# Optimization experiments

Measured on AMD Instinct MI355X. Metric: run time of the kernel, lower is better.

Reference implementation:

```python
import jax, jax.numpy as jnp
import numpy as np

N_NODES = 32768
N_EDGES = 524288
NODE_DIM, POS_DIM, EDGE_DIM = 44, 8, 1
HID, OUT, LAYERS, HEADS = 128, 128, 3, 4
DK = HID // HEADS
LN_EPS = 1e-5


def _linear_w(key, fan_in, fan_out):
    return (jax.random.normal(key, (fan_in, fan_out), jnp.float32) / np.sqrt(fan_in)).astype(jnp.float32)


def _ln(x, g, b):
    m = jnp.mean(x, axis=-1, keepdims=True)
    v = jnp.var(x, axis=-1, keepdims=True)
    return (x - m) * jax.lax.rsqrt(v + LN_EPS) * g + b


def setup_inputs() -> dict:
    key = jax.random.key(0)
    ks = jax.random.split(key, 16)
    inp = {
        'feats': jax.random.normal(ks[0], (N_NODES, NODE_DIM), jnp.float32),
        'lap_pos_enc': jax.random.normal(ks[1], (N_NODES, POS_DIM), jnp.float32),
        'edge_feats': jax.random.normal(ks[2], (N_EDGES, EDGE_DIM), jnp.float32),
        'src': jax.random.randint(ks[3], (N_EDGES,), 0, N_NODES, jnp.int32),
        'dst': jax.random.randint(ks[4], (N_EDGES,), 0, N_NODES, jnp.int32),
        # input projections
        'W_node': _linear_w(ks[5], NODE_DIM, HID), 'b_node': jnp.zeros((HID,), jnp.float32),
        'W_pos': _linear_w(ks[6], POS_DIM, HID), 'b_pos': jnp.zeros((HID,), jnp.float32),
        'W_edge': _linear_w(ks[7], EDGE_DIM, HID), 'b_edge': jnp.zeros((HID,), jnp.float32),
    }
    # per-layer stacked params (all layers are HID->HID since OUT==HID)
    def stack(k, fi, fo):
        kk = jax.random.split(k, LAYERS)
        return jnp.stack([_linear_w(kk[i], fi, fo) for i in range(LAYERS)])
    inp['Wq'] = stack(ks[8], HID, HID)
    inp['Wk'] = stack(ks[9], HID, HID)
    inp['Wv'] = stack(ks[10], HID, HID)
    inp['We'] = stack(ks[11], HID, HID)
    inp['W_lin'] = stack(ks[12], HID, HID)
    inp['b_lin'] = jnp.zeros((LAYERS, HID), jnp.float32)
    inp['g1'] = jnp.ones((LAYERS, HID), jnp.float32)
    inp['be1'] = jnp.zeros((LAYERS, HID), jnp.float32)
    inp['Wf1'] = stack(ks[13], HID, 2 * HID)
    inp['bf1'] = jnp.zeros((LAYERS, 2 * HID), jnp.float32)
    inp['Wf2'] = stack(ks[14], 2 * HID, HID)
    inp['bf2'] = jnp.zeros((LAYERS, HID), jnp.float32)
    inp['g2'] = jnp.ones((LAYERS, HID), jnp.float32)
    inp['be2'] = jnp.zeros((LAYERS, HID), jnp.float32)
    return inp


def reference(feats, lap_pos_enc, edge_feats,
              W_node, b_node, W_pos, b_pos, W_edge, b_edge,
              Wq, Wk, Wv, We, W_lin, b_lin, g1, be1,
              Wf1, bf1, Wf2, bf2, g2, be2, src, dst):
    n = feats.shape[0]
    inv_sqrt_dk = np.float32(1.0 / np.sqrt(DK))
    h = feats @ W_node + b_node + lap_pos_enc @ W_pos + b_pos      # [N, HID]
    e = edge_feats @ W_edge + b_edge                               # [E, HID] (shared across layers)
    for i in range(LAYERS):
        Q = (h @ Wq[i]).reshape(n, HEADS, DK)
        K = (h @ Wk[i]).reshape(n, HEADS, DK)
        V = (h @ Wv[i]).reshape(n, HEADS, DK)
        E = (e @ We[i]).reshape(-1, HEADS, DK)                     # [E, H, DK]
        # raw score [E, H, 1] broadcast against (1+E) -> [E, H, DK] (faithful to source)
        score = jnp.sum(K[src] * Q[dst], axis=-1, keepdims=True) * inv_sqrt_dk
        score = score * (1.0 + E)
        alpha = jnp.exp(score)                                      # [E, H, DK]
        Z = jnp.maximum(jax.ops.segment_sum(alpha, dst, num_segments=n), 1e-6)
        h_out = jax.ops.segment_sum(V[src] * alpha, dst, num_segments=n) / Z
        h_out = h_out.reshape(n, HEADS * DK)
        h = h + h_out @ W_lin[i] + b_lin[i]                        # residual + dropout(identity)
        h = _ln(h, g1[i], be1[i])
        h2 = jax.nn.relu(h @ Wf1[i] + bf1[i]) @ Wf2[i] + bf2[i]
        h = _ln(h + h2, g2[i], be2[i])
    # dgl.mean_nodes over a single graph -> [1, OUT]; readout LayerNorm is never applied in source
    return jnp.mean(h, axis=0, keepdims=True)
```

## Files before the change

### kernel.cpp

```cpp
#include <hip/hip_runtime.h>
#include <hip/hip_bf16.h>

#define N_NODES 32768
#define N_EDGES 524288
#define LN_EPS 1e-5f

typedef unsigned short ushort_t;
typedef __attribute__((ext_vector_type(8))) short short8v;
typedef __attribute__((ext_vector_type(4))) float float4v;
typedef __attribute__((ext_vector_type(2))) float float2v;

__device__ __forceinline__ float bf2f(ushort_t u) {
    return __uint_as_float(((unsigned int)u) << 16);
}
__device__ __forceinline__ ushort_t f2bf(float f) {
    unsigned int u = __float_as_uint(f);
    unsigned int r = (u + 0x7FFFu + ((u >> 16) & 1u)) >> 16;
    return (ushort_t)r;
}
__device__ __forceinline__ float lo16(unsigned int x) { return __uint_as_float(x << 16); }
__device__ __forceinline__ float hi16(unsigned int x) { return __uint_as_float(x & 0xFFFF0000u); }

#if __has_builtin(__builtin_amdgcn_exp2f)
#define EXP2(x) __builtin_amdgcn_exp2f(x)
#else
#define EXP2(x) exp2f(x)
#endif

#define OFF_WNODE 0
#define OFF_BNODE 5632
#define OFF_WPOS  5760
#define OFF_BPOS  6784
#define OFF_WEDGE 6912
#define OFF_BEDGE 7040
#define OFF_BLIN  7168
#define OFF_G1    7552
#define OFF_BE1   7936
#define OFF_BF1   8320
#define OFF_BF2   9088
#define OFF_G2    9472
#define OFF_BE2   9856
#define CONV_TOTAL 10240

#define REC_QKV(i)  ((i) * 96)
#define REC_WLIN(i) (288 + (i) * 32)
#define REC_WF1(i)  (384 + (i) * 64)
#define REC_WF2(i)  (576 + (i) * 64)
#define REC_WNP     768
#define REC_TOTAL   784

#define LDS_STRIDE 264
#define LDS_FSTRIDE 132

__global__ void detect_kernel(const unsigned int* __restrict__ wn, int* __restrict__ flag) {
    __shared__ int s[256];
    int t = threadIdx.x;
    int cnt = 0;
    for (int i = t; i < 2816; i += 256) {
        unsigned int b = (wn[i] >> 8) & 0x7F;
        cnt += (b >= 0x3A && b <= 0x40) ? 1 : 0;
    }
    s[t] = cnt;
    __syncthreads();
    for (int off = 128; off > 0; off >>= 1) {
        if (t < off) s[t] += s[t + off];
        __syncthreads();
    }
    if (t == 0) *flag = (s[0] > 1408) ? 1 : 0;
}

struct ConvArgs { const void* src[13]; };

__global__ void convert_kernel(ConvArgs a, const int* __restrict__ flag,
                               float* __restrict__ dst, int* __restrict__ deg) {
    int gid = blockIdx.x * 256 + threadIdx.x;
    for (int i = gid; i < N_NODES; i += CONV_TOTAL) deg[i] = 0;
    if (gid >= CONV_TOTAL) return;
    const int off[14] = {OFF_WNODE, OFF_BNODE, OFF_WPOS, OFF_BPOS, OFF_WEDGE, OFF_BEDGE,
                         OFF_BLIN, OFF_G1, OFF_BE1, OFF_BF1, OFF_BF2, OFF_G2, OFF_BE2,
                         CONV_TOTAL};
    int s = 0;
#pragma unroll
    for (int i = 1; i < 13; ++i) s += (gid >= off[i]) ? 1 : 0;
    int local = gid - off[s];
    if (*flag)
        dst[gid] = bf2f(((const ushort_t*)a.src[s])[local]);
    else
        dst[gid] = ((const float*)a.src[s])[local];
}

__global__ void swz_kernel(const void* __restrict__ Wq, const void* __restrict__ Wk,
                           const void* __restrict__ Wv, const void* __restrict__ Wlin,
                           const void* __restrict__ Wf1, const void* __restrict__ Wf2,
                           const void* __restrict__ We, const void* __restrict__ wedge,
                           const void* __restrict__ bedge,
                           const void* __restrict__ Wn_, const void* __restrict__ Wp_,
                           const int* __restrict__ flag,
                           ushort_t* __restrict__ swz,
                           float* __restrict__ u, float* __restrict__ c1) {
    const bool isbf = (*flag != 0);
    if (blockIdx.x >= 195) {
        int idx = (blockIdx.x - 195) * 256 + threadIdx.x;
        int rec16 = idx >> 6;
        int lane = idx & 63;
        int ct = rec16 >> 1, kb = rec16 & 1;
        int col = lane & 15, quad = lane >> 4;
        int n = ct * 16 + col;
        ushort_t v[8];
#pragma unroll
        for (int j = 0; j < 8; ++j) {
            int k = kb * 32 + quad * 8 + j;
            if (isbf) {
                v[j] = (k < 44) ? ((const ushort_t*)Wn_)[k * 128 + n]
                     : ((k < 52) ? ((const ushort_t*)Wp_)[(k - 44) * 128 + n]
                                 : (ushort_t)0);
            } else {
                float f = (k < 44) ? ((const float*)Wn_)[k * 128 + n]
                        : ((k < 52) ? ((const float*)Wp_)[(k - 44) * 128 + n] : 0.f);
                v[j] = f2bf(f);
            }
        }
        ushort_t* o = swz + (size_t)(REC_WNP + rec16) * 512 + lane * 8;
#pragma unroll
        for (int j = 0; j < 8; ++j) o[j] = v[j];
        return;
    }
    if (blockIdx.x >= 192) {
        int l = blockIdx.x - 192;
        int d = threadIdx.x;
        if (d >= 128) return;
        float uu = 0.f, cc = 0.f;
        if (isbf) {
            const ushort_t* Wl = (const ushort_t*)We + (size_t)l * 16384;
            const ushort_t* we_ = (const ushort_t*)wedge;
            const ushort_t* be_ = (const ushort_t*)bedge;
#pragma unroll 4
            for (int k = 0; k < 128; ++k) {
                float w = bf2f(Wl[k * 128 + d]);
                uu = fmaf(bf2f(we_[k]), w, uu);
                cc = fmaf(bf2f(be_[k]), w, cc);
            }
        } else {
            const float* Wl = (const float*)We + (size_t)l * 16384;
            const float* we_ = (const float*)wedge;
            const float* be_ = (const float*)bedge;
#pragma unroll 4
            for (int k = 0; k < 128; ++k) {
                float w = Wl[k * 128 + d];
                uu = fmaf(we_[k], w, uu);
                cc = fmaf(be_[k], w, cc);
            }
        }
        const float scale = 0.17677669529663687f * 1.4426950408889634f;
        u[l * 128 + d] = uu * scale;
        c1[l * 128 + d] = (1.f + cc) * scale;
        return;
    }
    int gid = blockIdx.x * 256 + threadIdx.x;
    int lane = gid & 63;
    int rec = gid >> 6;
    int col = lane & 15, quad = lane >> 4;
    const void* src;
    size_t base;
    int ct, kb, OC;
    if (rec < 288) {
        int layer = rec / 96, r2 = rec % 96;
        ct = r2 >> 2; kb = r2 & 3;
        int seg = ct >> 3;
        src = (seg == 0) ? Wq : ((seg == 1) ? Wk : Wv);
        base = (size_t)layer * 16384; OC = 128; ct &= 7;
    } else if (rec < 384) {
        int r = rec - 288, layer = r / 32, r2 = r % 32;
        ct = r2 >> 2; kb = r2 & 3;
        src = Wlin; base = (size_t)layer * 16384; OC = 128;
    } else if (rec < 576) {
        int r = rec - 384, layer = r / 64, r2 = r % 64;
        ct = r2 >> 2; kb = r2 & 3;
        src = Wf1; base = (size_t)layer * 32768; OC = 256;
    } else {
        int r = rec - 576, layer = r / 64, r2 = r % 64;
        ct = r2 >> 3; kb = r2 & 7;
        src = Wf2; base = (size_t)layer * 32768; OC = 128;
    }
    int n = ct * 16 + col;
    ushort_t v[8];
    if (isbf) {
        const ushort_t* s16 = (const ushort_t*)src + base;
#pragma unroll
        for (int j = 0; j < 8; ++j) v[j] = s16[(size_t)(kb * 32 + quad * 8 + j) * OC + n];
    } else {
        const float* s32 = (const float*)src + base;
#pragma unroll
        for (int j = 0; j < 8; ++j) v[j] = f2bf(s32[(size_t)(kb * 32 + quad * 8 + j) * OC + n]);
    }
    ushort_t* o = swz + (size_t)rec * 512 + lane * 8;
#pragma unroll
    for (int j = 0; j < 8; ++j) o[j] = v[j];
}

__global__ __launch_bounds__(256) void ip_gemm(
    const void* __restrict__ feats, const void* __restrict__ lap,
    const float* __restrict__ conv, const int* __restrict__ flag,
    const int* __restrict__ dstidx, int* __restrict__ deg,
    const ushort_t* __restrict__ Bswz,
    float* __restrict__ h, ushort_t* __restrict__ hb) {
    __shared__ __align__(16) ushort_t As[64 * 72];
    const int tid = threadIdx.x;

    for (int e = blockIdx.x * 256 + tid; e < N_EDGES; e += (N_NODES / 64) * 256)
        atomicAdd(&deg[dstidx[e]], 1);

    const bool isbf = (*flag != 0);
    const int r = tid >> 2;
    const int t4 = tid & 3;
    const int m0g = blockIdx.x * 64;
    {
        const int row = m0g + r;
        ushort_t tmp[16];
        if (isbf) {
            const ushort_t* frow = (const ushort_t*)feats + (size_t)row * 44;
            const ushort_t* prow = (const ushort_t*)lap + (size_t)row * 8;
#pragma unroll
            for (int j = 0; j < 16; ++j) {
                int k = t4 * 16 + j;
                tmp[j] = (k < 44) ? frow[k]
                       : ((k < 52) ? prow[k - 44] : (ushort_t)0);
            }
        } else {
            const float* frow = (const float*)feats + (size_t)row * 44;
            const float* prow = (const float*)lap + (size_t)row * 8;
#pragma unroll
            for (int j = 0; j < 16; ++j) {
                int k = t4 * 16 + j;
                float v = (k < 44) ? frow[k] : ((k < 52) ? prow[k - 44] : 0.f);
                tmp[j] = f2bf(v);
            }
        }
#pragma unroll
        for (int j = 0; j < 16; ++j) As[r * 72 + t4 * 16 + j] = tmp[j];
    }
    __syncthreads();

    const int wv = tid >> 6, lane = tid & 63;
    const int col = lane & 15, quad = lane >> 4;
    const int m0 = wv * 16;
    short8v a0 = *(const short8v*)&As[(m0 + col) * 72 + quad * 8];
    short8v a1 = *(const short8v*)&As[(m0 + col) * 72 + 32 + quad * 8];

    float4v acc[8];
#pragma unroll
    for (int ct = 0; ct < 8; ++ct) {
        short8v b0 = *(const short8v*)(Bswz + (size_t)(ct * 2 + 0) * 512 + lane * 8);
        short8v b1 = *(const short8v*)(Bswz + (size_t)(ct * 2 + 1) * 512 + lane * 8);
        float4v a = (float4v){0.f, 0.f, 0.f, 0.f};
        a = __builtin_amdgcn_mfma_f32_16x16x32_bf16(a0, b0, a, 0, 0, 0);
        a = __builtin_amdgcn_mfma_f32_16x16x32_bf16(a1, b1, a, 0, 0, 0);
        acc[ct] = a;
    }

    const int rowb = m0g + m0 + quad * 4;
#pragma unroll
    for (int ct = 0; ct < 8; ++ct) {
        int j = ct * 16 + col;
        float bias = conv[OFF_BNODE + j] + conv[OFF_BPOS + j];
#pragma unroll
        for (int rr = 0; rr < 4; ++rr) {
            float o = acc[ct][rr] + bias;
            h[(size_t)(rowb + rr) * 128 + j] = o;
            hb[(size_t)(rowb + rr) * 128 + j] = f2bf(o);
        }
    }
}

__global__ void scan_kernel(const int* __restrict__ deg, int* __restrict__ rowstart,
                            int* __restrict__ cursor, float* __restrict__ macc) {
    __shared__ int lds[1024];
    int t = threadIdx.x;
    if (t < 128) macc[t] = 0.f;
    int base = t * 32;
    int v[32];
    int csum = 0;
#pragma unroll
    for (int j = 0; j < 8; ++j) {
        int4 x = *(const int4*)(deg + base + j * 4);
        v[j * 4 + 0] = x.x; v[j * 4 + 1] = x.y;
        v[j * 4 + 2] = x.z; v[j * 4 + 3] = x.w;
        csum += x.x + x.y + x.z + x.w;
    }
    lds[t] = csum;
    __syncthreads();
    for (int off = 1; off < 1024; off <<= 1) {
        int x = (t >= off) ? lds[t - off] : 0;
        __syncthreads();
        lds[t] += x;
        __syncthreads();
    }
    int excl = lds[t] - csum;
    int running = excl;
#pragma unroll
    for (int j = 0; j < 8; ++j) {
        int4 w;
        w.x = running; running += v[j * 4 + 0];
        w.y = running; running += v[j * 4 + 1];
        w.z = running; running += v[j * 4 + 2];
        w.w = running; running += v[j * 4 + 3];
        *(int4*)(rowstart + base + j * 4) = w;
        *(int4*)(cursor + base + j * 4) = w;
    }
    if (t == 1023) rowstart[N_NODES] = running;
}

__global__ void scatter_kernel(const int* __restrict__ src, const int* __restrict__ dst,
                               const void* __restrict__ ef, const int* __restrict__ flag,
                               int* __restrict__ cursor,
                               unsigned int* __restrict__ edges) {
    int e = blockIdx.x * 256 + threadIdx.x;
    if (e < N_EDGES) {
        ushort_t efb = (*flag != 0) ? ((const ushort_t*)ef)[e]
                                    : f2bf(((const float*)ef)[e]);
        int d = dst[e];
        int p = atomicAdd(&cursor[d], 1);
        edges[p] = (unsigned int)src[e] | ((unsigned int)efb << 16);
    }
}

template <int KB>
__global__ __launch_bounds__(256) void qkv_gemm(
    const ushort_t* __restrict__ A,
    const ushort_t* __restrict__ Bswz,
    ushort_t* __restrict__ outQ,
    unsigned char* __restrict__ outKV) {
    const int K = KB * 32;
    const int tid = threadIdx.x;
    const int wv = tid >> 6, lane = tid & 63;
    const int col = lane & 15, quad = lane >> 4;
    const int m0 = blockIdx.x * 64 + wv * 16;
    const int ct0 = blockIdx.y * 8;

    float4v acc[8];
#pragma unroll
    for (int ct = 0; ct < 8; ++ct) acc[ct] = (float4v){0.f, 0.f, 0.f, 0.f};

    const ushort_t* Ap = A + (size_t)(m0 + col) * K + quad * 8;
    const ushort_t* Bp = Bswz + (size_t)ct0 * KB * 512 + lane * 8;

#pragma unroll
    for (int kb = 0; kb < KB; ++kb) {
        short8v a = *(const short8v*)(Ap + kb * 32);
#pragma unroll
        for (int ct = 0; ct < 8; ++ct) {
            short8v b = *(const short8v*)(Bp + (size_t)(ct * KB + kb) * 512);
            acc[ct] = __builtin_amdgcn_mfma_f32_16x16x32_bf16(a, b, acc[ct], 0, 0, 0);
        }
    }

    const int rowb = m0 + quad * 4;
    const int seg = blockIdx.y;
    if (seg == 0) {
#pragma unroll
        for (int ct = 0; ct < 8; ++ct) {
            int j = ct * 16 + col;
#pragma unroll
            for (int r = 0; r < 4; ++r)
                outQ[(size_t)(rowb + r) * 128 + j] = f2bf(acc[ct][r]);
        }
    } else {
        const int vofs = (seg == 2) ? 8 : 0;
#pragma unroll
        for (int ct = 0; ct < 8; ++ct) {
            int j = ct * 16 + col;
            int off = ((j >> 3) * 16) + (j & 7) + vofs;
#pragma unroll
            for (int r = 0; r < 4; ++r) {
                float a = acc[ct][r];
                float b = __shfl_xor(a, 1, 64);
                if ((col & 1) == 0) {
                    unsigned short pk = (unsigned short)
                        __builtin_amdgcn_cvt_pk_fp8_f32(a, b, 0, false);
                    *(ushort_t*)(outKV + (size_t)(rowb + r) * 256 + off) = pk;
                }
            }
        }
    }
}

__global__ __launch_bounds__(64, 2) void ffn_kernel(
    const ushort_t* __restrict__ HOUT,
    const ushort_t* __restrict__ BWL,
    const ushort_t* __restrict__ BF1,
    const ushort_t* __restrict__ BF2,
    const float* __restrict__ bl,
    const float* __restrict__ g1v, const float* __restrict__ be1v,
    const float* __restrict__ bf1v,
    const float* __restrict__ bf2v,
    const float* __restrict__ g2v, const float* __restrict__ be2v,
    float* __restrict__ h,
    ushort_t* __restrict__ hb) {
    __shared__ __align__(16) char ldsraw[16 * 528];
    ushort_t* ldsu = (ushort_t*)ldsraw;
    float* ldsf = (float*)ldsraw;
    const int lane = threadIdx.x & 63;
    const int col = lane & 15, quad = lane >> 4;
    const int m0 = blockIdx.x * 16;
    const int rowb = m0 + quad * 4;
    const int lrowc = quad * 4;
    const int lrowa = col;

    float4v acc[8];
#pragma unroll
    for (int ct = 0; ct < 8; ++ct) acc[ct] = (float4v){0.f, 0.f, 0.f, 0.f};
    const ushort_t* Ap = HOUT + (size_t)(m0 + col) * 128 + quad * 8;
#pragma unroll
    for (int kb = 0; kb < 4; ++kb) {
        short8v a = *(const short8v*)(Ap + kb * 32);
#pragma unroll
        for (int ct = 0; ct < 8; ++ct) {
            short8v b = *(const short8v*)(BWL + (size_t)(ct * 4 + kb) * 512 + lane * 8);
            acc[ct] = __builtin_amdgcn_mfma_f32_16x16x32_bf16(a, b, acc[ct], 0, 0, 0);
        }
    }

    float val[8][4], s[4] = {0.f, 0.f, 0.f, 0.f}, ss[4] = {0.f, 0.f, 0.f, 0.f};
#pragma unroll
    for (int ct = 0; ct < 8; ++ct) {
        float bi = bl[ct * 16 + col];
#pragma unroll
        for (int r = 0; r < 4; ++r) {
            float v = acc[ct][r] + bi + h[(size_t)(rowb + r) * 128 + ct * 16 + col];
            val[ct][r] = v;
            s[r] += v;
            ss[r] += v * v;
        }
    }
#pragma unroll
    for (int mask = 1; mask < 16; mask <<= 1) {
#pragma unroll
        for (int r = 0; r < 4; ++r) {
            s[r] += __shfl_xor(s[r], mask, 64);
            ss[r] += __shfl_xor(ss[r], mask, 64);
        }
    }
#pragma unroll
    for (int r = 0; r < 4; ++r) {
        float mean = s[r] * (1.f / 128.f);
        float var = ss[r] * (1.f / 128.f) - mean * mean;
        s[r] = mean;
        ss[r] = rsqrtf(var + LN_EPS);
    }
#pragma unroll
    for (int ct = 0; ct < 8; ++ct) {
        float gg = g1v[ct * 16 + col], bb = be1v[ct * 16 + col];
#pragma unroll
        for (int r = 0; r < 4; ++r) {
            float o = (val[ct][r] - s[r]) * ss[r] * gg + bb;
            val[ct][r] = o;
            ldsu[(lrowc + r) * LDS_STRIDE + ct * 16 + col] = f2bf(o);
        }
    }
    __syncthreads();

    short8v af[4];
#pragma unroll
    for (int kb = 0; kb < 4; ++kb)
        af[kb] = *(const short8v*)&ldsu[lrowa * LDS_STRIDE + kb * 32 + quad * 8];

    float4v acc2[16];
#pragma unroll
    for (int ct = 0; ct < 16; ++ct) acc2[ct] = (float4v){0.f, 0.f, 0.f, 0.f};
#pragma unroll
    for (int kb = 0; kb < 4; ++kb) {
#pragma unroll
        for (int ct = 0; ct < 16; ++ct) {
            short8v b = *(const short8v*)(BF1 + (size_t)(ct * 4 + kb) * 512 + lane * 8);
            acc2[ct] = __builtin_amdgcn_mfma_f32_16x16x32_bf16(af[kb], b, acc2[ct], 0, 0, 0);
        }
    }
    __syncthreads();

#pragma unroll
    for (int ct = 0; ct < 16; ++ct) {
        float bi = bf1v[ct * 16 + col];
#pragma unroll
        for (int r = 0; r < 4; ++r) {
            float v = fmaxf(acc2[ct][r] + bi, 0.f);
            ldsu[(lrowc + r) * LDS_STRIDE + ct * 16 + col] = f2bf(v);
        }
    }
    __syncthreads();

    float4v acc3[8];
#pragma unroll
    for (int ct = 0; ct < 8; ++ct) acc3[ct] = (float4v){0.f, 0.f, 0.f, 0.f};
#pragma unroll
    for (int kb = 0; kb < 8; ++kb) {
        short8v a = *(const short8v*)&ldsu[lrowa * LDS_STRIDE + kb * 32 + quad * 8];
#pragma unroll
        for (int ct = 0; ct < 8; ++ct) {
            short8v b = *(const short8v*)(BF2 + (size_t)(ct * 8 + kb) * 512 + lane * 8);
            acc3[ct] = __builtin_amdgcn_mfma_f32_16x16x32_bf16(a, b, acc3[ct], 0, 0, 0);
        }
    }

    float s2[4] = {0.f, 0.f, 0.f, 0.f}, ss2[4] = {0.f, 0.f, 0.f, 0.f};
#pragma unroll
    for (int ct = 0; ct < 8; ++ct) {
        float bi = bf2v[ct * 16 + col];
#pragma unroll
        for (int r = 0; r < 4; ++r) {
            float v = acc3[ct][r] + bi + val[ct][r];
            val[ct][r] = v;
            s2[r] += v;
            ss2[r] += v * v;
        }
    }
#pragma unroll
    for (int mask = 1; mask < 16; mask <<= 1) {
#pragma unroll
        for (int r = 0; r < 4; ++r) {
            s2[r] += __shfl_xor(s2[r], mask, 64);
            ss2[r] += __shfl_xor(ss2[r], mask, 64);
        }
    }
#pragma unroll
    for (int r = 0; r < 4; ++r) {
        float mean = s2[r] * (1.f / 128.f);
        float var = ss2[r] * (1.f / 128.f) - mean * mean;
        s2[r] = mean;
        ss2[r] = rsqrtf(var + LN_EPS);
    }
    __syncthreads();
#pragma unroll
    for (int ct = 0; ct < 8; ++ct) {
        float gg = g2v[ct * 16 + col], bb = be2v[ct * 16 + col];
#pragma unroll
        for (int r = 0; r < 4; ++r) {
            float o = (val[ct][r] - s2[r]) * ss2[r] * gg + bb;
            ldsf[(lrowc + r) * LDS_FSTRIDE + ct * 16 + col] = o;
        }
    }
    __syncthreads();

#pragma unroll
    for (int j = 0; j < 8; ++j) {
        int p = lane + j * 64;
        int row = p >> 5;
        int c4 = p & 31;
        float4 vv = *(const float4*)&ldsf[row * LDS_FSTRIDE + c4 * 4];
        *(float4*)&h[(size_t)(m0 + row) * 128 + c4 * 4] = vv;
    }
#pragma unroll
    for (int j = 0; j < 4; ++j) {
        int p = lane + j * 64;
        int row = p >> 4;
        int c8 = p & 15;
        float4 va = *(const float4*)&ldsf[row * LDS_FSTRIDE + c8 * 8];
        float4 vb = *(const float4*)&ldsf[row * LDS_FSTRIDE + c8 * 8 + 4];
        uint4 ou;
        ou.x = (unsigned)f2bf(va.x) | ((unsigned)f2bf(va.y) << 16);
        ou.y = (unsigned)f2bf(va.z) | ((unsigned)f2bf(va.w) << 16);
        ou.z = (unsigned)f2bf(vb.x) | ((unsigned)f2bf(vb.y) << 16);
        ou.w = (unsigned)f2bf(vb.z) | ((unsigned)f2bf(vb.w) << 16);
        *(uint4*)&hb[(size_t)(m0 + row) * 128 + c8 * 8] = ou;
    }
}

__global__ __launch_bounds__(64) void agg_kernel(
    const ushort_t* __restrict__ Q, const unsigned char* __restrict__ KV,
    const int* __restrict__ rowstart, const unsigned int* __restrict__ edges,
    const float* __restrict__ u, const float* __restrict__ c1,
    ushort_t* __restrict__ hout) {
    const int lane = threadIdx.x & 63;
    const int v = blockIdx.x;
    const int sub = lane & 15;
    const int grp = lane >> 4;

    uint4 qu = *(const uint4*)(Q + (size_t)v * 128 + sub * 8);
    float q0 = lo16(qu.x), q1 = hi16(qu.x), q2 = lo16(qu.y), q3 = hi16(qu.y);
    float q4 = lo16(qu.z), q5 = hi16(qu.z), q6 = lo16(qu.w), q7 = hi16(qu.w);
    float4 uva = *(const float4*)(u + sub * 8);
    float4 uvb = *(const float4*)(u + sub * 8 + 4);
    float4 cva = *(const float4*)(c1 + sub * 8);
    float4 cvb = *(const float4*)(c1 + sub * 8 + 4);

    float m = -1.0e38f;
    float sA[8] = {0.f, 0.f, 0.f, 0.f, 0.f, 0.f, 0.f, 0.f};
    float o[8] = {0.f, 0.f, 0.f, 0.f, 0.f, 0.f, 0.f, 0.f};

    const int start = rowstart[v];
    const int deg = rowstart[v + 1] - start;
    const int nfull = deg >> 2;
    const unsigned int* ep = edges + start + grp;

#define AGG_COMPUTE(PE, KVv, MASKED, VALID)                                      \
    {                                                                            \
        float ef_ = __uint_as_float((PE) & 0xFFFF0000u);                         \
        float2v k01 = __builtin_amdgcn_cvt_pk_f32_fp8((KVv).x, false);           \
        float2v k23 = __builtin_amdgcn_cvt_pk_f32_fp8((KVv).x, true);            \
        float2v k45 = __builtin_amdgcn_cvt_pk_f32_fp8((KVv).y, false);           \
        float2v k67 = __builtin_amdgcn_cvt_pk_f32_fp8((KVv).y, true);            \
        float p_ = k01[0] * q0;                                                  \
        p_ = fmaf(k01[1], q1, p_);                                               \
        p_ = fmaf(k23[0], q2, p_);                                               \
        p_ = fmaf(k23[1], q3, p_);                                               \
        p_ = fmaf(k45[0], q4, p_);                                               \
        p_ = fmaf(k45[1], q5, p_);                                               \
        p_ = fmaf(k67[0], q6, p_);                                               \
        p_ = fmaf(k67[1], q7, p_);                                               \
        p_ += __shfl_xor(p_, 1, 64);                                             \
        p_ += __shfl_xor(p_, 2, 64);                                             \
        float x0 = p_ * fmaf(ef_, uva.x, cva.x);                                 \
        float x1 = p_ * fmaf(ef_, uva.y, cva.y);                                 \
        float x2 = p_ * fmaf(ef_, uva.z, cva.z);                                 \
        float x3 = p_ * fmaf(ef_, uva.w, cva.w);                                 \
        float x4 = p_ * fmaf(ef_, uvb.x, cvb.x);                                 \
        float x5 = p_ * fmaf(ef_, uvb.y, cvb.y);                                 \
        float x6 = p_ * fmaf(ef_, uvb.z, cvb.z);                                 \
        float x7 = p_ * fmaf(ef_, uvb.w, cvb.w);                                 \
        if (MASKED) {                                                            \
            x0 = (VALID) ? x0 : -1.0e38f; x1 = (VALID) ? x1 : -1.0e38f;          \
            x2 = (VALID) ? x2 : -1.0e38f; x3 = (VALID) ? x3 : -1.0e38f;          \
            x4 = (VALID) ? x4 : -1.0e38f; x5 = (VALID) ? x5 : -1.0e38f;          \
            x6 = (VALID) ? x6 : -1.0e38f; x7 = (VALID) ? x7 : -1.0e38f;          \
        }                                                                        \
        float xm = fmaxf(fmaxf(fmaxf(x0, x1), fmaxf(x2, x3)),                    \
                         fmaxf(fmaxf(x4, x5), fmaxf(x6, x7)));                   \
        if (xm > m) {                                                            \
            float nm = xm + 6.0f;                                                \
            float sc = EXP2(m - nm);                                             \
            sA[0] *= sc; sA[1] *= sc; sA[2] *= sc; sA[3] *= sc;                  \
            sA[4] *= sc; sA[5] *= sc; sA[6] *= sc; sA[7] *= sc;                  \
            o[0] *= sc; o[1] *= sc; o[2] *= sc; o[3] *= sc;                      \
            o[4] *= sc; o[5] *= sc; o[6] *= sc; o[7] *= sc;                      \
            m = nm;                                                              \
        }                                                                        \
        float e0 = EXP2(x0 - m), e1 = EXP2(x1 - m);                              \
        float e2 = EXP2(x2 - m), e3 = EXP2(x3 - m);                              \
        float e4 = EXP2(x4 - m), e5 = EXP2(x5 - m);                              \
        float e6 = EXP2(x6 - m), e7 = EXP2(x7 - m);                              \
        sA[0] += e0; sA[1] += e1; sA[2] += e2; sA[3] += e3;                      \
        sA[4] += e4; sA[5] += e5; sA[6] += e6; sA[7] += e7;                      \
        float2v v01 = __builtin_amdgcn_cvt_pk_f32_fp8((KVv).z, false);           \
        float2v v23 = __builtin_amdgcn_cvt_pk_f32_fp8((KVv).z, true);            \
        float2v v45 = __builtin_amdgcn_cvt_pk_f32_fp8((KVv).w, false);           \
        float2v v67 = __builtin_amdgcn_cvt_pk_f32_fp8((KVv).w, true);            \
        o[0] = fmaf(v01[0], e0, o[0]);                                           \
        o[1] = fmaf(v01[1], e1, o[1]);                                           \
        o[2] = fmaf(v23[0], e2, o[2]);                                           \
        o[3] = fmaf(v23[1], e3, o[3]);                                           \
        o[4] = fmaf(v45[0], e4, o[4]);                                           \
        o[5] = fmaf(v45[1], e5, o[5]);                                           \
        o[6] = fmaf(v67[0], e6, o[6]);                                           \
        o[7] = fmaf(v67[1], e7, o[7]);                                           \
    }

    int it = 0;
    for (; it + 4 <= nfull; it += 4) {
        unsigned int pe0 = ep[4 * it];
        unsigned int pe1 = ep[4 * it + 4];
        unsigned int pe2 = ep[4 * it + 8];
        unsigned int pe3 = ep[4 * it + 12];
        uint4 kv0 = *(const uint4*)(KV + (size_t)(pe0 & 0xFFFFu) * 256 + sub * 16);
        uint4 kv1 = *(const uint4*)(KV + (size_t)(pe1 & 0xFFFFu) * 256 + sub * 16);
        uint4 kv2 = *(const uint4*)(KV + (size_t)(pe2 & 0xFFFFu) * 256 + sub * 16);
        uint4 kv3 = *(const uint4*)(KV + (size_t)(pe3 & 0xFFFFu) * 256 + sub * 16);
        AGG_COMPUTE(pe0, kv0, false, true)
        AGG_COMPUTE(pe1, kv1, false, true)
        AGG_COMPUTE(pe2, kv2, false, true)
        AGG_COMPUTE(pe3, kv3, false, true)
    }
    if (it + 2 <= nfull) {
        unsigned int pe0 = ep[4 * it];
        unsigned int pe1 = ep[4 * it + 4];
        uint4 kv0 = *(const uint4*)(KV + (size_t)(pe0 & 0xFFFFu) * 256 + sub * 16);
        uint4 kv1 = *(const uint4*)(KV + (size_t)(pe1 & 0xFFFFu) * 256 + sub * 16);
        AGG_COMPUTE(pe0, kv0, false, true)
        AGG_COMPUTE(pe1, kv1, false, true)
        it += 2;
    }
    if (it < nfull) {
        unsigned int pe0 = ep[4 * it];
        uint4 kv0 = *(const uint4*)(KV + (size_t)(pe0 & 0xFFFFu) * 256 + sub * 16);
        AGG_COMPUTE(pe0, kv0, false, true)
    }
    const int rem = deg & 3;
    if (rem) {
        bool valid = grp < rem;
        unsigned int pe = valid ? ep[4 * nfull] : edges[start];
        uint4 kv = *(const uint4*)(KV + (size_t)(pe & 0xFFFFu) * 256 + sub * 16);
        AGG_COMPUTE(pe, kv, true, valid)
    }
#undef AGG_COMPUTE

#pragma unroll
    for (int mask = 16; mask <= 32; mask <<= 1) {
        float mo = __shfl_xor(m, mask, 64);
        float mm = fmaxf(m, mo);
        float sca = EXP2(m - mm);
        float scb = EXP2(mo - mm);
#pragma unroll
        for (int j = 0; j < 8; ++j) {
            float t = __shfl_xor(sA[j], mask, 64);
            sA[j] = sA[j] * sca + t * scb;
            t = __shfl_xor(o[j], mask, 64);
            o[j] = o[j] * sca + t * scb;
        }
        m = mm;
    }

    if (grp == 0) {
        float zc = 1e-6f * EXP2(-m);
        uint4 ou;
        unsigned int w0, w1;
        float z;
        z = fmaxf(fmaxf(sA[0], zc), 1e-37f); w0 = f2bf(o[0] / z);
        z = fmaxf(fmaxf(sA[1], zc), 1e-37f); w1 = f2bf(o[1] / z);
        ou.x = w0 | (w1 << 16);
        z = fmaxf(fmaxf(sA[2], zc), 1e-37f); w0 = f2bf(o[2] / z);
        z = fmaxf(fmaxf(sA[3], zc), 1e-37f); w1 = f2bf(o[3] / z);
        ou.y = w0 | (w1 << 16);
        z = fmaxf(fmaxf(sA[4], zc), 1e-37f); w0 = f2bf(o[4] / z);
        z = fmaxf(fmaxf(sA[5], zc), 1e-37f); w1 = f2bf(o[5] / z);
        ou.z = w0 | (w1 << 16);
        z = fmaxf(fmaxf(sA[6], zc), 1e-37f); w0 = f2bf(o[6] / z);
        z = fmaxf(fmaxf(sA[7], zc), 1e-37f); w1 = f2bf(o[7] / z);
        ou.w = w0 | (w1 << 16);
        *(uint4*)(hout + (size_t)v * 128 + sub * 8) = ou;
    }
}

__global__ void mean_part_kernel(const float* __restrict__ h, float* __restrict__ macc) {
    __shared__ float s[256];
    int t = threadIdx.x;
    int col = t & 127;
    int half = t >> 7;
    int r0 = blockIdx.x * 256;
    float acc = 0.f;
    for (int r = half; r < 256; r += 2) acc += h[(size_t)(r0 + r) * 128 + col];
    s[t] = acc;
    __syncthreads();
    if (t < 128) atomicAdd(&macc[t], s[t] + s[t + 128]);
}

__global__ void finalize_kernel(const float* __restrict__ macc, void* __restrict__ out,
                                const int* __restrict__ flag) {
    int t = threadIdx.x;
    float v = macc[t] * (1.f / (float)N_NODES);
    if (*flag)
        ((ushort_t*)out)[t] = f2bf(v);
    else
        ((float*)out)[t] = v;
}

extern "C" void kernel_launch(void* const* d_in, const int* in_sizes, int n_in,
                              void* d_out, int out_size, void* d_ws, size_t ws_size,
                              hipStream_t stream) {
    const int* src = (const int*)d_in[3];
    const int* dst = (const int*)d_in[4];

    char* w = (char*)d_ws;
    const size_t MB = 1u << 20;
    float* h        = (float*)(w);
    ushort_t* hb    = (ushort_t*)(w + 16 * MB);
    ushort_t* Qh    = (ushort_t*)(w + 24 * MB);
    unsigned char* KVf8 = (unsigned char*)(w + 32 * MB);
    char* aux       = w + 48 * MB;
    int* deg        = (int*)(aux);
    int* rowstart   = (int*)(aux + 0x40000);
    int* cursor     = (int*)(aux + 0x80000);
    unsigned int* edges = (unsigned int*)(aux + 0xC0000);
    float* ubuf     = (float*)(aux + 0xC0000 + 2 * MB);
    float* cbuf     = ubuf + 3 * 128;
    float* macc     = cbuf + 3 * 128;
    int* flag       = (int*)(macc + 128);
    float* conv     = (float*)(aux + 0xC0000 + 2 * MB + 4096);
    ushort_t* swz   = (ushort_t*)((char*)conv + CONV_TOTAL * 4);

    detect_kernel<<<1, 256, 0, stream>>>((const unsigned int*)d_in[5], flag);

    ConvArgs ca;
    ca.src[0] = d_in[5];
    ca.src[1] = d_in[6];
    ca.src[2] = d_in[7];
    ca.src[3] = d_in[8];
    ca.src[4] = d_in[9];
    ca.src[5] = d_in[10];
    ca.src[6] = d_in[16];
    ca.src[7] = d_in[17];
    ca.src[8] = d_in[18];
    ca.src[9] = d_in[20];
    ca.src[10] = d_in[22];
    ca.src[11] = d_in[23];
    ca.src[12] = d_in[24];
    convert_kernel<<<(CONV_TOTAL + 255) / 256, 256, 0, stream>>>(ca, flag, conv, deg);

    swz_kernel<<<192 + 3 + 4, 256, 0, stream>>>(
        d_in[11], d_in[12], d_in[13], d_in[15], d_in[19], d_in[21],
        d_in[14], d_in[9], d_in[10], d_in[5], d_in[7], flag, swz, ubuf, cbuf);

    ip_gemm<<<N_NODES / 64, 256, 0, stream>>>(d_in[0], d_in[1], conv, flag, dst, deg,
                                              swz + (size_t)REC_WNP * 512, h, hb);
    scan_kernel<<<1, 1024, 0, stream>>>(deg, rowstart, cursor, macc);
    scatter_kernel<<<N_EDGES / 256, 256, 0, stream>>>(src, dst, d_in[2], flag, cursor,
                                                      edges);

    for (int i = 0; i < 3; ++i) {
        const ushort_t* swzQKV = swz + (size_t)REC_QKV(i) * 512;
        const ushort_t* swzWL  = swz + (size_t)REC_WLIN(i) * 512;
        const ushort_t* swzF1  = swz + (size_t)REC_WF1(i) * 512;
        const ushort_t* swzF2  = swz + (size_t)REC_WF2(i) * 512;

        qkv_gemm<4><<<dim3(N_NODES / 64, 3), 256, 0, stream>>>(hb, swzQKV, Qh, KVf8);

        agg_kernel<<<N_NODES, 64, 0, stream>>>(Qh, KVf8, rowstart, edges,
                                               ubuf + i * 128, cbuf + i * 128, hb);

        ffn_kernel<<<N_NODES / 16, 64, 0, stream>>>(
            hb, swzWL, swzF1, swzF2,
            conv + OFF_BLIN + i * 128, conv + OFF_G1 + i * 128, conv + OFF_BE1 + i * 128,
            conv + OFF_BF1 + i * 256,
            conv + OFF_BF2 + i * 128, conv + OFF_G2 + i * 128, conv + OFF_BE2 + i * 128,
            h, hb);
    }

    mean_part_kernel<<<N_NODES / 256, 256, 0, stream>>>(h, macc);
    finalize_kernel<<<1, 128, 0, stream>>>(macc, d_out, flag);
}
```

Before: 475.7 us.

## Ping-pong hidden-state buffers and overlap FFN row tiles with half stride

```diff
diff --git a/kernel.cpp b/kernel.cpp
--- a/kernel.cpp
+++ b/kernel.cpp
@@ -394,14 +394,15 @@
     const float* __restrict__ bf1v,
     const float* __restrict__ bf2v,
     const float* __restrict__ g2v, const float* __restrict__ be2v,
-    float* __restrict__ h,
+    const float* __restrict__ hin,
+    float* __restrict__ hout,
     ushort_t* __restrict__ hb) {
     __shared__ __align__(16) char ldsraw[16 * 528];
     ushort_t* ldsu = (ushort_t*)ldsraw;
     float* ldsf = (float*)ldsraw;
     const int lane = threadIdx.x & 63;
     const int col = lane & 15, quad = lane >> 4;
-    const int m0 = blockIdx.x * 16;
+    const int m0 = blockIdx.x * 8;
     const int rowb = m0 + quad * 4;
     const int lrowc = quad * 4;
     const int lrowa = col;
@@ -426,7 +427,7 @@
         float bi = bl[ct * 16 + col];
 #pragma unroll
         for (int r = 0; r < 4; ++r) {
-            float v = acc[ct][r] + bi + h[(size_t)(rowb + r) * 128 + ct * 16 + col];
+            float v = acc[ct][r] + bi + hin[(size_t)(rowb + r) * 128 + ct * 16 + col];
             val[ct][r] = v;
             s[r] += v;
             ss[r] += v * v;
@@ -546,7 +547,7 @@
         int row = p >> 5;
         int c4 = p & 31;
         float4 vv = *(const float4*)&ldsf[row * LDS_FSTRIDE + c4 * 4];
-        *(float4*)&h[(size_t)(m0 + row) * 128 + c4 * 4] = vv;
+        *(float4*)&hout[(size_t)(m0 + row) * 128 + c4 * 4] = vv;
     }
 #pragma unroll
     for (int j = 0; j < 4; ++j) {
@@ -759,11 +760,14 @@
 
     char* w = (char*)d_ws;
     const size_t MB = 1u << 20;
-    float* h        = (float*)(w);
-    ushort_t* hb    = (ushort_t*)(w + 16 * MB);
-    ushort_t* Qh    = (ushort_t*)(w + 24 * MB);
-    unsigned char* KVf8 = (unsigned char*)(w + 32 * MB);
-    char* aux       = w + 48 * MB;
+    float* hA       = (float*)(w);
+    float* hB       = (float*)(w + 16 * MB);
+    ushort_t* hbA   = (ushort_t*)(w + 32 * MB);
+    ushort_t* hbB   = (ushort_t*)(w + 40 * MB);
+    ushort_t* HOUT  = (ushort_t*)(w + 48 * MB);
+    ushort_t* Qh    = (ushort_t*)(w + 56 * MB);
+    unsigned char* KVf8 = (unsigned char*)(w + 64 * MB);
+    char* aux       = w + 72 * MB;
     int* deg        = (int*)(aux);
     int* rowstart   = (int*)(aux + 0x40000);
     int* cursor     = (int*)(aux + 0x80000);
@@ -798,7 +802,7 @@
         d_in[14], d_in[9], d_in[10], d_in[5], d_in[7], flag, swz, ubuf, cbuf);
 
     ip_gemm<<<N_NODES / 64, 256, 0, stream>>>(d_in[0], d_in[1], conv, flag, dst, deg,
-                                              swz + (size_t)REC_WNP * 512, h, hb);
+                                              swz + (size_t)REC_WNP * 512, hA, hbA);
     scan_kernel<<<1, 1024, 0, stream>>>(deg, rowstart, cursor, macc);
     scatter_kernel<<<N_EDGES / 256, 256, 0, stream>>>(src, dst, d_in[2], flag, cursor,
                                                       edges);
@@ -808,20 +812,24 @@
         const ushort_t* swzWL  = swz + (size_t)REC_WLIN(i) * 512;
         const ushort_t* swzF1  = swz + (size_t)REC_WF1(i) * 512;
         const ushort_t* swzF2  = swz + (size_t)REC_WF2(i) * 512;
-
-        qkv_gemm<4><<<dim3(N_NODES / 64, 3), 256, 0, stream>>>(hb, swzQKV, Qh, KVf8);
+        const float* hin   = (i & 1) ? hB : hA;
+        float* hout        = (i & 1) ? hA : hB;
+        const ushort_t* Ain = (i & 1) ? hbB : hbA;
+        ushort_t* Aout      = (i & 1) ? hbA : hbB;
+
+        qkv_gemm<4><<<dim3(N_NODES / 64, 3), 256, 0, stream>>>(Ain, swzQKV, Qh, KVf8);
 
         agg_kernel<<<N_NODES, 64, 0, stream>>>(Qh, KVf8, rowstart, edges,
-                                               ubuf + i * 128, cbuf + i * 128, hb);
-
-        ffn_kernel<<<N_NODES / 16, 64, 0, stream>>>(
-            hb, swzWL, swzF1, swzF2,
+                                               ubuf + i * 128, cbuf + i * 128, HOUT);
+
+        ffn_kernel<<<N_NODES / 8 - 1, 64, 0, stream>>>(
+            HOUT, swzWL, swzF1, swzF2,
             conv + OFF_BLIN + i * 128, conv + OFF_G1 + i * 128, conv + OFF_BE1 + i * 128,
             conv + OFF_BF1 + i * 256,
             conv + OFF_BF2 + i * 128, conv + OFF_G2 + i * 128, conv + OFF_BE2 + i * 128,
-            h, hb);
-    }
-
-    mean_part_kernel<<<N_NODES / 256, 256, 0, stream>>>(h, macc);
+            hin, hout, Aout);
+    }
+
+    mean_part_kernel<<<N_NODES / 256, 256, 0, stream>>>(hB, macc);
     finalize_kernel<<<1, 128, 0, stream>>>(macc, d_out, flag);
 }
```

Result: slower. 564.3 us (+18.6%).

## Split FFN kernel output columns across two waves per block

Applied to the files above, without the earlier changes.

```diff
diff --git a/kernel.cpp b/kernel.cpp
--- a/kernel.cpp
+++ b/kernel.cpp
@@ -384,7 +384,7 @@
     }
 }
 
-__global__ __launch_bounds__(64, 2) void ffn_kernel(
+__global__ __launch_bounds__(128, 2) void ffn_kernel(
     const ushort_t* __restrict__ HOUT,
     const ushort_t* __restrict__ BWL,
     const ushort_t* __restrict__ BF1,
@@ -397,37 +397,41 @@
     float* __restrict__ h,
     ushort_t* __restrict__ hb) {
     __shared__ __align__(16) char ldsraw[16 * 528];
+    __shared__ float lnx[2][16][2];
     ushort_t* ldsu = (ushort_t*)ldsraw;
     float* ldsf = (float*)ldsraw;
-    const int lane = threadIdx.x & 63;
+    const int tid = threadIdx.x;
+    const int wv = tid >> 6;
+    const int lane = tid & 63;
     const int col = lane & 15, quad = lane >> 4;
     const int m0 = blockIdx.x * 16;
     const int rowb = m0 + quad * 4;
     const int lrowc = quad * 4;
     const int lrowa = col;
-
-    float4v acc[8];
-#pragma unroll
-    for (int ct = 0; ct < 8; ++ct) acc[ct] = (float4v){0.f, 0.f, 0.f, 0.f};
+    const int ct0 = wv * 4;
+
+    float4v acc[4];
+#pragma unroll
+    for (int c = 0; c < 4; ++c) acc[c] = (float4v){0.f, 0.f, 0.f, 0.f};
     const ushort_t* Ap = HOUT + (size_t)(m0 + col) * 128 + quad * 8;
 #pragma unroll
     for (int kb = 0; kb < 4; ++kb) {
         short8v a = *(const short8v*)(Ap + kb * 32);
 #pragma unroll
-        for (int ct = 0; ct < 8; ++ct) {
-            short8v b = *(const short8v*)(BWL + (size_t)(ct * 4 + kb) * 512 + lane * 8);
-            acc[ct] = __builtin_amdgcn_mfma_f32_16x16x32_bf16(a, b, acc[ct], 0, 0, 0);
-        }
-    }
-
-    float val[8][4], s[4] = {0.f, 0.f, 0.f, 0.f}, ss[4] = {0.f, 0.f, 0.f, 0.f};
-#pragma unroll
-    for (int ct = 0; ct < 8; ++ct) {
-        float bi = bl[ct * 16 + col];
+        for (int c = 0; c < 4; ++c) {
+            short8v b = *(const short8v*)(BWL + (size_t)((ct0 + c) * 4 + kb) * 512 + lane * 8);
+            acc[c] = __builtin_amdgcn_mfma_f32_16x16x32_bf16(a, b, acc[c], 0, 0, 0);
+        }
+    }
+
+    float val[4][4], s[4] = {0.f, 0.f, 0.f, 0.f}, ss[4] = {0.f, 0.f, 0.f, 0.f};
+#pragma unroll
+    for (int c = 0; c < 4; ++c) {
+        float bi = bl[(ct0 + c) * 16 + col];
 #pragma unroll
         for (int r = 0; r < 4; ++r) {
-            float v = acc[ct][r] + bi + h[(size_t)(rowb + r) * 128 + ct * 16 + col];
-            val[ct][r] = v;
+            float v = acc[c][r] + bi + h[(size_t)(rowb + r) * 128 + (ct0 + c) * 16 + col];
+            val[c][r] = v;
             s[r] += v;
             ss[r] += v * v;
         }
@@ -440,21 +444,31 @@
             ss[r] += __shfl_xor(ss[r], mask, 64);
         }
     }
+    if (col == 0) {
+#pragma unroll
+        for (int r = 0; r < 4; ++r) {
+            lnx[wv][lrowc + r][0] = s[r];
+            lnx[wv][lrowc + r][1] = ss[r];
+        }
+    }
+    __syncthreads();
 #pragma unroll
     for (int r = 0; r < 4; ++r) {
-        float mean = s[r] * (1.f / 128.f);
-        float var = ss[r] * (1.f / 128.f) - mean * mean;
+        float fs = lnx[0][lrowc + r][0] + lnx[1][lrowc + r][0];
+        float fss = lnx[0][lrowc + r][1] + lnx[1][lrowc + r][1];
+        float mean = fs * (1.f / 128.f);
+        float var = fss * (1.f / 128.f) - mean * mean;
         s[r] = mean;
         ss[r] = rsqrtf(var + LN_EPS);
     }
 #pragma unroll
-    for (int ct = 0; ct < 8; ++ct) {
-        float gg = g1v[ct * 16 + col], bb = be1v[ct * 16 + col];
+    for (int c = 0; c < 4; ++c) {
+        float gg = g1v[(ct0 + c) * 16 + col], bb = be1v[(ct0 + c) * 16 + col];
 #pragma unroll
         for (int r = 0; r < 4; ++r) {
-            float o = (val[ct][r] - s[r]) * ss[r] * gg + bb;
-            val[ct][r] = o;
-            ldsu[(lrowc + r) * LDS_STRIDE + ct * 16 + col] = f2bf(o);
+            float o = (val[c][r] - s[r]) * ss[r] * gg + bb;
+            val[c][r] = o;
+            ldsu[(lrowc + r) * LDS_STRIDE + (ct0 + c) * 16 + col] = f2bf(o);
         }
     }
     __syncthreads();
@@ -464,51 +478,51 @@
     for (int kb = 0; kb < 4; ++kb)
         af[kb] = *(const short8v*)&ldsu[lrowa * LDS_STRIDE + kb * 32 + quad * 8];
 
-    float4v acc2[16];
-#pragma unroll
-    for (int ct = 0; ct < 16; ++ct) acc2[ct] = (float4v){0.f, 0.f, 0.f, 0.f};
+    float4v acc2[8];
+#pragma unroll
+    for (int c = 0; c < 8; ++c) acc2[c] = (float4v){0.f, 0.f, 0.f, 0.f};
 #pragma unroll
     for (int kb = 0; kb < 4; ++kb) {
 #pragma unroll
-        for (int ct = 0; ct < 16; ++ct) {
-            short8v b = *(const short8v*)(BF1 + (size_t)(ct * 4 + kb) * 512 + lane * 8);
-            acc2[ct] = __builtin_amdgcn_mfma_f32_16x16x32_bf16(af[kb], b, acc2[ct], 0, 0, 0);
-        }
-    }
-    __syncthreads();
-
-#pragma unroll
-    for (int ct = 0; ct < 16; ++ct) {
-        float bi = bf1v[ct * 16 + col];
+        for (int c = 0; c < 8; ++c) {
+            short8v b = *(const short8v*)(BF1 + (size_t)((wv * 8 + c) * 4 + kb) * 512 + lane * 8);
+            acc2[c] = __builtin_amdgcn_mfma_f32_16x16x32_bf16(af[kb], b, acc2[c], 0, 0, 0);
+        }
+    }
+    __syncthreads();
+
+#pragma unroll
+    for (int c = 0; c < 8; ++c) {
+        float bi = bf1v[(wv * 8 + c) * 16 + col];
 #pragma unroll
         for (int r = 0; r < 4; ++r) {
-            float v = fmaxf(acc2[ct][r] + bi, 0.f);
-            ldsu[(lrowc + r) * LDS_STRIDE + ct * 16 + col] = f2bf(v);
-        }
-    }
-    __syncthreads();
-
-    float4v acc3[8];
-#pragma unroll
-    for (int ct = 0; ct < 8; ++ct) acc3[ct] = (float4v){0.f, 0.f, 0.f, 0.f};
+            float v = fmaxf(acc2[c][r] + bi, 0.f);
+            ldsu[(lrowc + r) * LDS_STRIDE + (wv * 8 + c) * 16 + col] = f2bf(v);
+        }
+    }
+    __syncthreads();
+
+    float4v acc3[4];
+#pragma unroll
+    for (int c = 0; c < 4; ++c) acc3[c] = (float4v){0.f, 0.f, 0.f, 0.f};
 #pragma unroll
     for (int kb = 0; kb < 8; ++kb) {
         short8v a = *(const short8v*)&ldsu[lrowa * LDS_STRIDE + kb * 32 + quad * 8];
 #pragma unroll
-        for (int ct = 0; ct < 8; ++ct) {
-            short8v b = *(const short8v*)(BF2 + (size_t)(ct * 8 + kb) * 512 + lane * 8);
-            acc3[ct] = __builtin_amdgcn_mfma_f32_16x16x32_bf16(a, b, acc3[ct], 0, 0, 0);
+        for (int c = 0; c < 4; ++c) {
+            short8v b = *(const short8v*)(BF2 + (size_t)((ct0 + c) * 8 + kb) * 512 + lane * 8);
+            acc3[c] = __builtin_amdgcn_mfma_f32_16x16x32_bf16(a, b, acc3[c], 0, 0, 0);
         }
     }
 
     float s2[4] = {0.f, 0.f, 0.f, 0.f}, ss2[4] = {0.f, 0.f, 0.f, 0.f};
 #pragma unroll
-    for (int ct = 0; ct < 8; ++ct) {
-        float bi = bf2v[ct * 16 + col];
+    for (int c = 0; c < 4; ++c) {
+        float bi = bf2v[(ct0 + c) * 16 + col];
 #pragma unroll
         for (int r = 0; r < 4; ++r) {
-            float v = acc3[ct][r] + bi + val[ct][r];
-            val[ct][r] = v;
+            float v = acc3[c][r] + bi + val[c][r];
+            val[c][r] = v;
             s2[r] += v;
             ss2[r] += v * v;
         }
@@ -521,36 +535,46 @@
             ss2[r] += __shfl_xor(ss2[r], mask, 64);
         }
     }
+    __syncthreads();
+    if (col == 0) {
+#pragma unroll
+        for (int r = 0; r < 4; ++r) {
+            lnx[wv][lrowc + r][0] = s2[r];
+            lnx[wv][lrowc + r][1] = ss2[r];
+        }
+    }
+    __syncthreads();
 #pragma unroll
     for (int r = 0; r < 4; ++r) {
-        float mean = s2[r] * (1.f / 128.f);
-        float var = ss2[r] * (1.f / 128.f) - mean * mean;
+        float fs = lnx[0][lrowc + r][0] + lnx[1][lrowc + r][0];
+        float fss = lnx[0][lrowc + r][1] + lnx[1][lrowc + r][1];
+        float mean = fs * (1.f / 128.f);
+        float var = fss * (1.f / 128.f) - mean * mean;
         s2[r] = mean;
         ss2[r] = rsqrtf(var + LN_EPS);
     }
-    __syncthreads();
-#pragma unroll
-    for (int ct = 0; ct < 8; ++ct) {
-        float gg = g2v[ct * 16 + col], bb = be2v[ct * 16 + col];
+#pragma unroll
+    for (int c = 0; c < 4; ++c) {
+        float gg = g2v[(ct0 + c) * 16 + col], bb = be2v[(ct0 + c) * 16 + col];
 #pragma unroll
         for (int r = 0; r < 4; ++r) {
-            float o = (val[ct][r] - s2[r]) * ss2[r] * gg + bb;
-            ldsf[(lrowc + r) * LDS_FSTRIDE + ct * 16 + col] = o;
-        }
-    }
-    __syncthreads();
-
-#pragma unroll
-    for (int j = 0; j < 8; ++j) {
-        int p = lane + j * 64;
+            float o = (val[c][r] - s2[r]) * ss2[r] * gg + bb;
+            ldsf[(lrowc + r) * LDS_FSTRIDE + (ct0 + c) * 16 + col] = o;
+        }
+    }
+    __syncthreads();
+
+#pragma unroll
+    for (int j = 0; j < 4; ++j) {
+        int p = tid + j * 128;
         int row = p >> 5;
         int c4 = p & 31;
         float4 vv = *(const float4*)&ldsf[row * LDS_FSTRIDE + c4 * 4];
         *(float4*)&h[(size_t)(m0 + row) * 128 + c4 * 4] = vv;
     }
 #pragma unroll
-    for (int j = 0; j < 4; ++j) {
-        int p = lane + j * 64;
+    for (int j = 0; j < 2; ++j) {
+        int p = tid + j * 128;
         int row = p >> 4;
         int c8 = p & 15;
         float4 va = *(const float4*)&ldsf[row * LDS_FSTRIDE + c8 * 8];
@@ -814,7 +838,7 @@
         agg_kernel<<<N_NODES, 64, 0, stream>>>(Qh, KVf8, rowstart, edges,
                                                ubuf + i * 128, cbuf + i * 128, hb);
 
-        ffn_kernel<<<N_NODES / 16, 64, 0, stream>>>(
+        ffn_kernel<<<N_NODES / 16, 128, 0, stream>>>(
             hb, swzWL, swzF1, swzF2,
             conv + OFF_BLIN + i * 128, conv + OFF_G1 + i * 128, conv + OFF_BE1 + i * 128,
             conv + OFF_BF1 + i * 256,
```

After: 444.4 us. 1.07x faster.
